# Kernel tuning notes

Hardware: AMD Instinct MI355X
Metric: run time of the kernel (lower is better)

The kernel has to match this reference:

```python
import jax, jax.numpy as jnp
import numpy as np

B, L, H, E = 4, 2048, 16, 64  # batch, seq, heads, head_dim (S=L, D=E)


def setup_inputs() -> dict:
    key = jax.random.key(0)
    kq, kk, kv = jax.random.split(key, 3)
    queries = jax.random.normal(kq, (B, L, H, E), dtype=jnp.float32)
    keys = jax.random.normal(kk, (B, L, H, E), dtype=jnp.float32)
    values = jax.random.normal(kv, (B, L, H, E), dtype=jnp.float32)
    return {"queries": queries, "keys": keys, "values": values}


def reference(queries, keys, values):
    Bq, Lq, Hq, Eq = queries.shape
    scale = 1.0 / float(np.sqrt(Eq))
    # scores: [B, H, L, S]
    scores = jnp.einsum('blhe,bshe->bhls', queries, keys)
    # causal mask: forbid attending to future positions (strict upper triangle)
    causal = jnp.triu(jnp.ones((Lq, Lq), dtype=bool), k=1)
    scores = jnp.where(causal[None, None, :, :], -jnp.inf, scores)
    A = jax.nn.softmax(scale * scores, axis=-1)  # dropout p=0 -> identity
    V = jnp.einsum('bhls,bshd->blhd', A, values)  # [B, L, H, D]
    return V
```

## Files before the change

kernel.cpp:

```cpp
#include <hip/hip_runtime.h>
#include <hip/hip_bf16.h>

typedef short bs8 __attribute__((ext_vector_type(8)));
typedef short bs4 __attribute__((ext_vector_type(4)));
typedef float f32x4 __attribute__((ext_vector_type(4)));

#define B_ 4
#define L_ 2048
#define H_ 16
#define E_ 64
#define QT_ 64
#define KT_ 64
#define KSTR 72
#define PSTR 76
#define NEG_INF (-1e30f)
#define SCALE_LOG2E (0.125f * 1.44269504088896340736f)

__device__ __forceinline__ short bf16of(float x) {
  __hip_bfloat16 h = __float2bfloat16(x);
  return *reinterpret_cast<short*>(&h);
}

__global__ __launch_bounds__(256) void prep(const float* __restrict__ K,
                                            const float* __restrict__ V,
                                            short* __restrict__ Kb,
                                            short* __restrict__ Vt) {
  __shared__ unsigned int lt[64 * 35];
  const int tid = threadIdx.x;
  if (blockIdx.x < 1024) {
    size_t base = (size_t)blockIdx.x * 256 + tid;
#pragma unroll
    for (int i = 0; i < 8; ++i) {
      size_t g = base + (size_t)i * 262144;
      int e4 = g & 15;
      int h  = (g >> 4) & 15;
      int s  = (g >> 8) & 2047;
      int b  = (int)(g >> 19);
      float4 v = *(const float4*)(K + g * 4);
      bs4 o;
      o.x = bf16of(v.x); o.y = bf16of(v.y); o.z = bf16of(v.z); o.w = bf16of(v.w);
      *(bs4*)(Kb + (((size_t)(b * 16 + h) * L_ + s) * E_ + e4 * 4)) = o;
    }
  } else {
    int vb = blockIdx.x - 1024;
    int st = vb & 31, bh = vb >> 5;
    int b = bh >> 4, h = bh & 15;
    int s0 = st * 64;
#pragma unroll
    for (int i = 0; i < 2; ++i) {
      int idx = i * 256 + tid;
      int sp = idx >> 4;
      int e4 = idx & 15;
      const float* p0 = V + (((size_t)b * L_ + s0 + 2 * sp) * H_ + h) * E_ + e4 * 4;
      float4 v0 = *(const float4*)p0;
      float4 v1 = *(const float4*)(p0 + H_ * E_);
      unsigned u;
      u = (unsigned short)bf16of(v0.x) | ((unsigned)(unsigned short)bf16of(v1.x) << 16);
      lt[(e4 * 4 + 0) * 35 + sp] = u;
      u = (unsigned short)bf16of(v0.y) | ((unsigned)(unsigned short)bf16of(v1.y) << 16);
      lt[(e4 * 4 + 1) * 35 + sp] = u;
      u = (unsigned short)bf16of(v0.z) | ((unsigned)(unsigned short)bf16of(v1.z) << 16);
      lt[(e4 * 4 + 2) * 35 + sp] = u;
      u = (unsigned short)bf16of(v0.w) | ((unsigned)(unsigned short)bf16of(v1.w) << 16);
      lt[(e4 * 4 + 3) * 35 + sp] = u;
    }
    __syncthreads();
#pragma unroll
    for (int i = 0; i < 2; ++i) {
      int idx = i * 256 + tid;
      int e  = idx >> 3;
      int s8 = idx & 7;
      uint4 o;
      o.x = lt[e * 35 + s8 * 4 + 0];
      o.y = lt[e * 35 + s8 * 4 + 1];
      o.z = lt[e * 35 + s8 * 4 + 2];
      o.w = lt[e * 35 + s8 * 4 + 3];
      *(uint4*)(Vt + ((size_t)bh * E_ + e) * L_ + s0 + 8 * s8) = o;
    }
  }
}

__global__ __launch_bounds__(256, 4) void flash_fwd(const float* __restrict__ Q,
                                                    const short* __restrict__ Kb,
                                                    const short* __restrict__ Vt,
                                                    float* __restrict__ O) {
  const int id = blockIdx.x;
  const int slot = id >> 3;
  const int bh = (id & 7) * 8 + (slot >> 4);
  const int p  = slot & 15;
  const int b = bh >> 4, h = bh & 15;
  const int tid = threadIdx.x;
  const int w = tid >> 6;
  const int lane = tid & 63;
  const int quad = lane >> 4;
  const int l16 = lane & 15;

  __shared__ short ldsK[KT_ * KSTR];
  __shared__ short ldsV[E_ * KSTR];
  __shared__ short ldsP[QT_ * PSTR];

  const short* KbBase = Kb + (size_t)bh * L_ * E_;
  const short* VtBase = Vt + (size_t)bh * E_ * L_;

  const int sr = tid >> 3;
  const int sc = (tid & 7) * 8;

  bs8 bOne;
  {
    short one = (l16 == 0) ? (short)0x3F80 : (short)0;
#pragma unroll
    for (int j = 0; j < 8; ++j) bOne[j] = one;
  }

  for (int phase = 0; phase < 2; ++phase) {
    const int qt = phase ? (31 - p) : p;
    const int q0 = qt * QT_;
    const int nkt = qt + 1;

    bs8 aQ[2];
    {
      const int q = q0 + w * 16 + l16;
      const float* qp = Q + (((size_t)b * L_ + q) * H_ + h) * E_ + quad * 8;
#pragma unroll
      for (int c = 0; c < 2; ++c) {
        float4 f0 = *(const float4*)(qp + c * 32);
        float4 f1 = *(const float4*)(qp + c * 32 + 4);
        bs8 a;
        a[0] = bf16of(f0.x * SCALE_LOG2E); a[1] = bf16of(f0.y * SCALE_LOG2E);
        a[2] = bf16of(f0.z * SCALE_LOG2E); a[3] = bf16of(f0.w * SCALE_LOG2E);
        a[4] = bf16of(f1.x * SCALE_LOG2E); a[5] = bf16of(f1.y * SCALE_LOG2E);
        a[6] = bf16of(f1.z * SCALE_LOG2E); a[7] = bf16of(f1.w * SCALE_LOG2E);
        aQ[c] = a;
      }
    }

    f32x4 accO[4];
    f32x4 accL = (f32x4){0.f, 0.f, 0.f, 0.f};
#pragma unroll
    for (int nt = 0; nt < 4; ++nt) accO[nt] = (f32x4){0.f, 0.f, 0.f, 0.f};

    bs8 pfK[2], pfV[2];
#pragma unroll
    for (int i = 0; i < 2; ++i) {
      pfK[i] = *(const bs8*)(KbBase + (size_t)(sr + 32 * i) * E_ + sc);
      pfV[i] = *(const bs8*)(VtBase + (size_t)(sr + 32 * i) * L_ + sc);
    }

    for (int kt = 0; kt < nkt; ++kt) {
      const int k0 = kt * KT_;
      __syncthreads();

#pragma unroll
      for (int i = 0; i < 2; ++i) {
        *(bs8*)&ldsK[(sr + 32 * i) * KSTR + sc] = pfK[i];
        *(bs8*)&ldsV[(sr + 32 * i) * KSTR + sc] = pfV[i];
      }
      if (kt + 1 < nkt) {
        const int kn = k0 + KT_;
#pragma unroll
        for (int i = 0; i < 2; ++i) {
          pfK[i] = *(const bs8*)(KbBase + (size_t)(kn + sr + 32 * i) * E_ + sc);
          pfV[i] = *(const bs8*)(VtBase + (size_t)(sr + 32 * i) * L_ + kn + sc);
        }
      }
      __syncthreads();

      f32x4 sA[4];
#pragma unroll
      for (int nt = 0; nt < 4; ++nt) {
        bs8 bK0 = *(const bs8*)&ldsK[(nt * 16 + l16) * KSTR + quad * 8];
        bs8 bK1 = *(const bs8*)&ldsK[(nt * 16 + l16) * KSTR + 32 + quad * 8];
        f32x4 acc = (f32x4){0.f, 0.f, 0.f, 0.f};
        acc = __builtin_amdgcn_mfma_f32_16x16x32_bf16(aQ[0], bK0, acc, 0, 0, 0);
        acc = __builtin_amdgcn_mfma_f32_16x16x32_bf16(aQ[1], bK1, acc, 0, 0, 0);
        sA[nt] = acc;
      }

      if (kt == nkt - 1) {
        const int qb = q0 + w * 16 + quad * 4;
#pragma unroll
        for (int nt = 0; nt < 4; ++nt) {
          int key = k0 + nt * 16 + l16;
#pragma unroll
          for (int r = 0; r < 4; ++r)
            if (key > qb + r) sA[nt][r] = NEG_INF;
        }
      }

      {
        const int rowb = w * 16 + quad * 4;
#pragma unroll
        for (int nt = 0; nt < 4; ++nt)
#pragma unroll
          for (int r = 0; r < 4; ++r)
            ldsP[(rowb + r) * PSTR + nt * 16 + l16] = bf16of(exp2f(sA[nt][r]));
      }

      __threadfence_block();

      bs8 aP[2];
      {
        const int rowa = w * 16 + l16;
#pragma unroll
        for (int c = 0; c < 2; ++c)
          aP[c] = *(const bs8*)&ldsP[rowa * PSTR + c * 32 + quad * 8];
        accL = __builtin_amdgcn_mfma_f32_16x16x32_bf16(aP[0], bOne, accL, 0, 0, 0);
        accL = __builtin_amdgcn_mfma_f32_16x16x32_bf16(aP[1], bOne, accL, 0, 0, 0);
      }
#pragma unroll
      for (int nt = 0; nt < 4; ++nt) {
        bs8 bV0 = *(const bs8*)&ldsV[(nt * 16 + l16) * KSTR + quad * 8];
        bs8 bV1 = *(const bs8*)&ldsV[(nt * 16 + l16) * KSTR + 32 + quad * 8];
        accO[nt] = __builtin_amdgcn_mfma_f32_16x16x32_bf16(aP[0], bV0, accO[nt], 0, 0, 0);
        accO[nt] = __builtin_amdgcn_mfma_f32_16x16x32_bf16(aP[1], bV1, accO[nt], 0, 0, 0);
      }
    }

    {
      float inv[4];
#pragma unroll
      for (int r = 0; r < 4; ++r)
        inv[r] = 1.f / __shfl(accL[r], lane & 48, 64);
#pragma unroll
      for (int nt = 0; nt < 4; ++nt) {
        const int q = q0 + w * 16 + quad * 4;
        const int d = nt * 16 + l16;
        float* op = O + (((size_t)b * L_ + q) * H_ + h) * E_ + d;
#pragma unroll
        for (int r = 0; r < 4; ++r)
          op[(size_t)r * H_ * E_] = accO[nt][r] * inv[r];
      }
    }
  }
}

extern "C" void kernel_launch(void* const* d_in, const int* in_sizes, int n_in,
                              void* d_out, int out_size, void* d_ws, size_t ws_size,
                              hipStream_t stream) {
  (void)in_sizes; (void)n_in; (void)out_size; (void)ws_size;
  const float* Q = (const float*)d_in[0];
  const float* K = (const float*)d_in[1];
  const float* V = (const float*)d_in[2];
  float* Out = (float*)d_out;
  short* Kb = (short*)d_ws;
  short* Vt = Kb + (size_t)B_ * H_ * L_ * E_;

  prep<<<1024 + 2048, 256, 0, stream>>>(K, V, Kb, Vt);
  flash_fwd<<<1024, 256, 0, stream>>>(Q, Kb, Vt, Out);
}
```

Baseline: 206.1 us.

## Switch attention to 32x32 MFMA with transposed scores and register-resident P

Rewrites the flash kernel to compute S^T with 32x32x16 bf16 MFMAs so each wave owns 32 queries in a 128-row tile. The probabilities are repacked in registers with v_permlane32_swap instead of a round trip through LDS, and the row sum is accumulated with plain VALU adds instead of a ones-vector MFMA. Each block now handles a single 128-query tile, ordered largest first, in place of the previous paired-phase balancing, and output is staged through LDS for coalesced float4 stores. The goal is to cut LDS traffic and MFMA issue count, at the cost of coarser load balance, waves idling on skipped tiles, and occupancy lowered to 3 blocks.

```diff
diff --git a/kernel.cpp b/kernel.cpp
--- a/kernel.cpp
+++ b/kernel.cpp
@@ -4,15 +4,16 @@
 typedef short bs8 __attribute__((ext_vector_type(8)));
 typedef short bs4 __attribute__((ext_vector_type(4)));
 typedef float f32x4 __attribute__((ext_vector_type(4)));
+typedef float f32x16 __attribute__((ext_vector_type(16)));
+typedef int i32x4 __attribute__((ext_vector_type(4)));
 
 #define B_ 4
 #define L_ 2048
 #define H_ 16
 #define E_ 64
-#define QT_ 64
 #define KT_ 64
 #define KSTR 72
-#define PSTR 76
+#define SCSTR 68
 #define NEG_INF (-1e30f)
 #define SCALE_LOG2E (0.125f * 1.44269504088896340736f)
 
@@ -80,157 +81,162 @@
   }
 }
 
-__global__ __launch_bounds__(256, 4) void flash_fwd(const float* __restrict__ Q,
+__global__ __launch_bounds__(256, 3) void flash_fwd(const float* __restrict__ Q,
                                                     const short* __restrict__ Kb,
                                                     const short* __restrict__ Vt,
                                                     float* __restrict__ O) {
-  const int id = blockIdx.x;
-  const int slot = id >> 3;
-  const int bh = (id & 7) * 8 + (slot >> 4);
-  const int p  = slot & 15;
+  const int id  = blockIdx.x;
+  const int xcd = id & 7;
+  const int j   = id >> 3;
+  const int qt  = 15 - (j & 15);
+  const int bh  = xcd * 8 + (j >> 4);
   const int b = bh >> 4, h = bh & 15;
   const int tid = threadIdx.x;
   const int w = tid >> 6;
   const int lane = tid & 63;
-  const int quad = lane >> 4;
-  const int l16 = lane & 15;
-
-  __shared__ short ldsK[KT_ * KSTR];
-  __shared__ short ldsV[E_ * KSTR];
-  __shared__ short ldsP[QT_ * PSTR];
+  const int l32 = lane & 31;
+  const int hh  = lane >> 5;
+  const int h8  = hh * 8;
+
+  __shared__ __align__(16) char smem[4 * 32 * SCSTR * 4];
+  short* ldsK = (short*)smem;
+  short* ldsV = (short*)(smem + KT_ * KSTR * 2);
 
   const short* KbBase = Kb + (size_t)bh * L_ * E_;
   const short* VtBase = Vt + (size_t)bh * E_ * L_;
 
+  const int q0w = qt * 128 + w * 32;
+  const int nkt = 2 * (qt + 1);
+
   const int sr = tid >> 3;
-  const int sc = (tid & 7) * 8;
-
-  bs8 bOne;
+  const int sc8 = (tid & 7) * 8;
+
+  bs8 aQ[4];
   {
-    short one = (l16 == 0) ? (short)0x3F80 : (short)0;
-#pragma unroll
-    for (int j = 0; j < 8; ++j) bOne[j] = one;
-  }
-
-  for (int phase = 0; phase < 2; ++phase) {
-    const int qt = phase ? (31 - p) : p;
-    const int q0 = qt * QT_;
-    const int nkt = qt + 1;
-
-    bs8 aQ[2];
-    {
-      const int q = q0 + w * 16 + l16;
-      const float* qp = Q + (((size_t)b * L_ + q) * H_ + h) * E_ + quad * 8;
-#pragma unroll
-      for (int c = 0; c < 2; ++c) {
-        float4 f0 = *(const float4*)(qp + c * 32);
-        float4 f1 = *(const float4*)(qp + c * 32 + 4);
-        bs8 a;
-        a[0] = bf16of(f0.x * SCALE_LOG2E); a[1] = bf16of(f0.y * SCALE_LOG2E);
-        a[2] = bf16of(f0.z * SCALE_LOG2E); a[3] = bf16of(f0.w * SCALE_LOG2E);
-        a[4] = bf16of(f1.x * SCALE_LOG2E); a[5] = bf16of(f1.y * SCALE_LOG2E);
-        a[6] = bf16of(f1.z * SCALE_LOG2E); a[7] = bf16of(f1.w * SCALE_LOG2E);
-        aQ[c] = a;
-      }
-    }
-
-    f32x4 accO[4];
-    f32x4 accL = (f32x4){0.f, 0.f, 0.f, 0.f};
-#pragma unroll
-    for (int nt = 0; nt < 4; ++nt) accO[nt] = (f32x4){0.f, 0.f, 0.f, 0.f};
-
-    bs8 pfK[2], pfV[2];
+    const float* qp = Q + (((size_t)b * L_ + q0w + l32) * H_ + h) * E_ + h8;
+#pragma unroll
+    for (int ks = 0; ks < 4; ++ks) {
+      float4 f0 = *(const float4*)(qp + ks * 16);
+      float4 f1 = *(const float4*)(qp + ks * 16 + 4);
+      bs8 a;
+      a[0] = bf16of(f0.x * SCALE_LOG2E); a[1] = bf16of(f0.y * SCALE_LOG2E);
+      a[2] = bf16of(f0.z * SCALE_LOG2E); a[3] = bf16of(f0.w * SCALE_LOG2E);
+      a[4] = bf16of(f1.x * SCALE_LOG2E); a[5] = bf16of(f1.y * SCALE_LOG2E);
+      a[6] = bf16of(f1.z * SCALE_LOG2E); a[7] = bf16of(f1.w * SCALE_LOG2E);
+      aQ[ks] = a;
+    }
+  }
+
+  f32x16 accO[2];
+#pragma unroll
+  for (int d = 0; d < 2; ++d)
+#pragma unroll
+    for (int r = 0; r < 16; ++r) accO[d][r] = 0.f;
+  float accL = 0.f;
+
+  bs8 pfK[2], pfV[2];
+#pragma unroll
+  for (int i = 0; i < 2; ++i) {
+    pfK[i] = *(const bs8*)(KbBase + (size_t)(sr + 32 * i) * E_ + sc8);
+    pfV[i] = *(const bs8*)(VtBase + (size_t)(sr + 32 * i) * L_ + sc8);
+  }
+
+  for (int kt = 0; kt < nkt; ++kt) {
+    const int k0 = kt * KT_;
+    __syncthreads();
 #pragma unroll
     for (int i = 0; i < 2; ++i) {
-      pfK[i] = *(const bs8*)(KbBase + (size_t)(sr + 32 * i) * E_ + sc);
-      pfV[i] = *(const bs8*)(VtBase + (size_t)(sr + 32 * i) * L_ + sc);
-    }
-
-    for (int kt = 0; kt < nkt; ++kt) {
-      const int k0 = kt * KT_;
-      __syncthreads();
-
+      *(bs8*)&ldsK[(sr + 32 * i) * KSTR + sc8] = pfK[i];
+      *(bs8*)&ldsV[(sr + 32 * i) * KSTR + sc8] = pfV[i];
+    }
+    if (kt + 1 < nkt) {
+      const int kn = k0 + KT_;
 #pragma unroll
       for (int i = 0; i < 2; ++i) {
-        *(bs8*)&ldsK[(sr + 32 * i) * KSTR + sc] = pfK[i];
-        *(bs8*)&ldsV[(sr + 32 * i) * KSTR + sc] = pfV[i];
-      }
-      if (kt + 1 < nkt) {
-        const int kn = k0 + KT_;
-#pragma unroll
-        for (int i = 0; i < 2; ++i) {
-          pfK[i] = *(const bs8*)(KbBase + (size_t)(kn + sr + 32 * i) * E_ + sc);
-          pfV[i] = *(const bs8*)(VtBase + (size_t)(sr + 32 * i) * L_ + kn + sc);
+        pfK[i] = *(const bs8*)(KbBase + (size_t)(kn + sr + 32 * i) * E_ + sc8);
+        pfV[i] = *(const bs8*)(VtBase + (size_t)(sr + 32 * i) * L_ + kn + sc8);
+      }
+    }
+    __syncthreads();
+
+    if (k0 > q0w + 31) continue;
+    const bool diag = (k0 + KT_ - 1 > q0w);
+
+    bs8 pB[2][2];
+#pragma unroll
+    for (int sub = 0; sub < 2; ++sub) {
+      f32x16 cc;
+#pragma unroll
+      for (int r = 0; r < 16; ++r) cc[r] = 0.f;
+#pragma unroll
+      for (int ks = 0; ks < 4; ++ks) {
+        bs8 aK = *(const bs8*)&ldsK[(sub * 32 + l32) * KSTR + ks * 16 + h8];
+        cc = __builtin_amdgcn_mfma_f32_32x32x16_bf16(aK, aQ[ks], cc, 0, 0, 0);
+      }
+      if (diag) {
+        const int qcol = q0w + l32;
+#pragma unroll
+        for (int r = 0; r < 16; ++r) {
+          const int key = k0 + sub * 32 + ((r & 3) + 8 * (r >> 2) + 4 * hh);
+          if (key > qcol) cc[r] = NEG_INF;
         }
       }
-      __syncthreads();
-
-      f32x4 sA[4];
-#pragma unroll
-      for (int nt = 0; nt < 4; ++nt) {
-        bs8 bK0 = *(const bs8*)&ldsK[(nt * 16 + l16) * KSTR + quad * 8];
-        bs8 bK1 = *(const bs8*)&ldsK[(nt * 16 + l16) * KSTR + 32 + quad * 8];
-        f32x4 acc = (f32x4){0.f, 0.f, 0.f, 0.f};
-        acc = __builtin_amdgcn_mfma_f32_16x16x32_bf16(aQ[0], bK0, acc, 0, 0, 0);
-        acc = __builtin_amdgcn_mfma_f32_16x16x32_bf16(aQ[1], bK1, acc, 0, 0, 0);
-        sA[nt] = acc;
-      }
-
-      if (kt == nkt - 1) {
-        const int qb = q0 + w * 16 + quad * 4;
-#pragma unroll
-        for (int nt = 0; nt < 4; ++nt) {
-          int key = k0 + nt * 16 + l16;
-#pragma unroll
-          for (int r = 0; r < 4; ++r)
-            if (key > qb + r) sA[nt][r] = NEG_INF;
+      float p[16];
+#pragma unroll
+      for (int r = 0; r < 16; ++r) p[r] = exp2f(cc[r]);
+      accL += ((((p[0] + p[1]) + (p[2] + p[3])) + ((p[4] + p[5]) + (p[6] + p[7]))) +
+               (((p[8] + p[9]) + (p[10] + p[11])) + ((p[12] + p[13]) + (p[14] + p[15]))));
+      unsigned pk[8];
+#pragma unroll
+      for (int i = 0; i < 8; ++i)
+        pk[i] = (unsigned)(unsigned short)bf16of(p[2 * i]) |
+                ((unsigned)(unsigned short)bf16of(p[2 * i + 1]) << 16);
+      unsigned w0 = pk[0], w2 = pk[2];
+      asm("v_permlane32_swap_b32 %0, %1" : "+v"(w0), "+v"(w2));
+      unsigned w1 = pk[1], w3 = pk[3];
+      asm("v_permlane32_swap_b32 %0, %1" : "+v"(w1), "+v"(w3));
+      unsigned w4 = pk[4], w6 = pk[6];
+      asm("v_permlane32_swap_b32 %0, %1" : "+v"(w4), "+v"(w6));
+      unsigned w5 = pk[5], w7 = pk[7];
+      asm("v_permlane32_swap_b32 %0, %1" : "+v"(w5), "+v"(w7));
+      i32x4 f0 = {(int)w0, (int)w1, (int)w2, (int)w3};
+      i32x4 f1 = {(int)w4, (int)w5, (int)w6, (int)w7};
+      pB[sub][0] = *(bs8*)&f0;
+      pB[sub][1] = *(bs8*)&f1;
+    }
+
+#pragma unroll
+    for (int dsub = 0; dsub < 2; ++dsub) {
+#pragma unroll
+      for (int sub = 0; sub < 2; ++sub) {
+#pragma unroll
+        for (int ks = 0; ks < 2; ++ks) {
+          bs8 aV = *(const bs8*)&ldsV[(dsub * 32 + l32) * KSTR + sub * 32 + ks * 16 + h8];
+          accO[dsub] = __builtin_amdgcn_mfma_f32_32x32x16_bf16(aV, pB[sub][ks], accO[dsub], 0, 0, 0);
         }
       }
-
-      {
-        const int rowb = w * 16 + quad * 4;
-#pragma unroll
-        for (int nt = 0; nt < 4; ++nt)
-#pragma unroll
-          for (int r = 0; r < 4; ++r)
-            ldsP[(rowb + r) * PSTR + nt * 16 + l16] = bf16of(exp2f(sA[nt][r]));
-      }
-
-      __threadfence_block();
-
-      bs8 aP[2];
-      {
-        const int rowa = w * 16 + l16;
-#pragma unroll
-        for (int c = 0; c < 2; ++c)
-          aP[c] = *(const bs8*)&ldsP[rowa * PSTR + c * 32 + quad * 8];
-        accL = __builtin_amdgcn_mfma_f32_16x16x32_bf16(aP[0], bOne, accL, 0, 0, 0);
-        accL = __builtin_amdgcn_mfma_f32_16x16x32_bf16(aP[1], bOne, accL, 0, 0, 0);
-      }
-#pragma unroll
-      for (int nt = 0; nt < 4; ++nt) {
-        bs8 bV0 = *(const bs8*)&ldsV[(nt * 16 + l16) * KSTR + quad * 8];
-        bs8 bV1 = *(const bs8*)&ldsV[(nt * 16 + l16) * KSTR + 32 + quad * 8];
-        accO[nt] = __builtin_amdgcn_mfma_f32_16x16x32_bf16(aP[0], bV0, accO[nt], 0, 0, 0);
-        accO[nt] = __builtin_amdgcn_mfma_f32_16x16x32_bf16(aP[1], bV1, accO[nt], 0, 0, 0);
-      }
-    }
-
-    {
-      float inv[4];
-#pragma unroll
-      for (int r = 0; r < 4; ++r)
-        inv[r] = 1.f / __shfl(accL[r], lane & 48, 64);
-#pragma unroll
-      for (int nt = 0; nt < 4; ++nt) {
-        const int q = q0 + w * 16 + quad * 4;
-        const int d = nt * 16 + l16;
-        float* op = O + (((size_t)b * L_ + q) * H_ + h) * E_ + d;
-#pragma unroll
-        for (int r = 0; r < 4; ++r)
-          op[(size_t)r * H_ * E_] = accO[nt][r] * inv[r];
-      }
-    }
+    }
+  }
+
+  const float inv = 1.f / (accL + __shfl_xor(accL, 32, 64));
+
+  __syncthreads();
+  float* scb = (float*)(smem + w * (32 * SCSTR * 4));
+#pragma unroll
+  for (int dsub = 0; dsub < 2; ++dsub)
+#pragma unroll
+    for (int g = 0; g < 4; ++g) {
+      f32x4 vv = {accO[dsub][4 * g + 0] * inv, accO[dsub][4 * g + 1] * inv,
+                  accO[dsub][4 * g + 2] * inv, accO[dsub][4 * g + 3] * inv};
+      *(f32x4*)&scb[(size_t)l32 * SCSTR + dsub * 32 + 8 * g + 4 * hh] = vv;
+    }
+#pragma unroll
+  for (int jj = 0; jj < 8; ++jj) {
+    const int qq = jj * 4 + (lane >> 4);
+    const int d0 = (lane & 15) * 4;
+    f32x4 ov = *(const f32x4*)&scb[(size_t)qq * SCSTR + d0];
+    float* op = O + (((size_t)b * L_ + q0w + qq) * H_ + h) * E_ + d0;
+    *(f32x4*)op = ov;
   }
 }
 
```

New measurement: 205.5 us. Within noise of the previous version (-0.3%).
